# Kernel tuning notes

Measured on AMD Instinct MI355X. Metric: run time of the kernel, lower is better.

## Reference

```python
import jax, jax.numpy as jnp
import numpy as np

H, B, M, D = 2, 2048, 64, 16
N_ENT, N_REL = 500000, 32


def setup_inputs() -> dict:
    key = jax.random.key(0)
    k1, k2, k3, k4, k5, k6 = jax.random.split(key, 6)
    items = jax.random.randint(k1, (B,), 0, N_ENT)
    heads = jax.random.randint(k2, (H, B, M), 0, N_ENT)
    relations = jax.random.randint(k3, (H, B, M), 0, N_REL)
    tails = jax.random.randint(k4, (H, B, M), 0, N_ENT)
    ent_emb = jax.random.normal(k5, (N_ENT, D), dtype=jnp.float32) * 0.1
    rel_emb = jax.random.normal(k6, (N_REL, D, D), dtype=jnp.float32) * 0.1
    return {"items": items, "heads": heads, "relations": relations,
            "tails": tails, "ent_emb": ent_emb, "rel_emb": rel_emb}


def reference(items, heads, relations, tails, ent_emb, rel_emb):
    # gathers over ragged-as-dense ripple sets
    item_e = ent_emb[items]        # [B, D]
    head_e = ent_emb[heads]        # [H, B, M, D]
    rel_e = rel_emb[relations]     # [H, B, M, D, D]
    tail_e = ent_emb[tails]        # [H, B, M, D]
    # Rh = R @ h  -> [H, B, M, D]
    Rh = jnp.einsum('hbmij,hbmj->hbmi', rel_e, head_e)
    # attention logits hRv = Rh . v (item embedding) -> [H, B, M]
    hRv = jnp.einsum('hbmi,bi->hbm', Rh, item_e)
    pi = jax.nn.softmax(hRv, axis=2)          # softmax over memory dim (dim=1 in torch per hop)
    # weighted tail aggregation, summed over hops -> [B, D]
    user_rep = jnp.einsum('hbm,hbmd->bd', pi, tail_e)
    predicts = jax.nn.sigmoid(jnp.sum(user_rep * item_e, axis=1))  # [B]
    return predicts
```

## Files before the change

### kernel.cpp

```cpp
#include <hip/hip_runtime.h>
#include <math.h>

#define HOPS 2
#define BATCH 2048
#define MEM 64
#define DIM 16
#define NREL 32
#define RSTRIDE 20

__global__ __launch_bounds__(512)
void ripple_kernel(const int* __restrict__ items,
                   const int* __restrict__ heads,
                   const int* __restrict__ relations,
                   const int* __restrict__ tails,
                   const float* __restrict__ ent_emb,
                   const float* __restrict__ rel_emb,
                   float* __restrict__ out)
{
    const int b    = blockIdx.x;
    const int tid  = threadIdx.x;
    const int sub  = tid & 3;
    const int g    = tid >> 2;
    const int h    = g >> 6;
    const int m    = g & 63;
    const int wave = tid >> 6;

    __shared__ float s_itemR[NREL * RSTRIDE];
    __shared__ float s_num[8];
    __shared__ float s_den[8];

    const int base = h * (BATCH * MEM) + b * MEM + m;
    const int hidx = heads[base];
    const int ridx = relations[base];
    const int tidx = tails[base];

    const float4* ip = (const float4*)(ent_emb + (size_t)items[b] * DIM);
    const float4 it0 = ip[0], it1 = ip[1], it2 = ip[2], it3 = ip[3];

    const float4 hseg = *(const float4*)(ent_emb + (size_t)hidx * DIM + sub * 4);
    const float4 tseg = *(const float4*)(ent_emb + (size_t)tidx * DIM + sub * 4);

    {
        const int r = tid >> 4;
        const int j = tid & 15;
        const float* Rp = rel_emb + r * (DIM * DIM) + j;
        float acc;
        acc = it0.x * Rp[0];
        acc = fmaf(it0.y, Rp[16],  acc);
        acc = fmaf(it0.z, Rp[32],  acc);
        acc = fmaf(it0.w, Rp[48],  acc);
        acc = fmaf(it1.x, Rp[64],  acc);
        acc = fmaf(it1.y, Rp[80],  acc);
        acc = fmaf(it1.z, Rp[96],  acc);
        acc = fmaf(it1.w, Rp[112], acc);
        acc = fmaf(it2.x, Rp[128], acc);
        acc = fmaf(it2.y, Rp[144], acc);
        acc = fmaf(it2.z, Rp[160], acc);
        acc = fmaf(it2.w, Rp[176], acc);
        acc = fmaf(it3.x, Rp[192], acc);
        acc = fmaf(it3.y, Rp[208], acc);
        acc = fmaf(it3.z, Rp[224], acc);
        acc = fmaf(it3.w, Rp[240], acc);
        s_itemR[r * RSTRIDE + j] = acc;
    }
    __syncthreads();

    const float4 irseg = *(const float4*)(s_itemR + ridx * RSTRIDE + sub * 4);
    const float4 iseg  = (sub == 0) ? it0 : (sub == 1) ? it1
                       : (sub == 2) ? it2 : it3;

    float lpart = hseg.x * irseg.x + hseg.y * irseg.y +
                  hseg.z * irseg.z + hseg.w * irseg.w;
    float tpart = tseg.x * iseg.x + tseg.y * iseg.y +
                  tseg.z * iseg.z + tseg.w * iseg.w;

    lpart += __shfl_xor(lpart, 1, 64);
    lpart += __shfl_xor(lpart, 2, 64);

    const float e = __expf(lpart);
    float num = e * tpart;
    float den = e * 0.25f;
    #pragma unroll
    for (int off = 1; off < 64; off <<= 1) {
        num += __shfl_xor(num, off, 64);
        den += __shfl_xor(den, off, 64);
    }
    if ((tid & 63) == 0) { s_num[wave] = num; s_den[wave] = den; }
    __syncthreads();

    if (tid == 0) {
        const float n0 = s_num[0] + s_num[1] + s_num[2] + s_num[3];
        const float d0 = s_den[0] + s_den[1] + s_den[2] + s_den[3];
        const float n1 = s_num[4] + s_num[5] + s_num[6] + s_num[7];
        const float d1 = s_den[4] + s_den[5] + s_den[6] + s_den[7];
        const float x = n0 / d0 + n1 / d1;
        out[b] = 1.0f / (1.0f + __expf(-x));
    }
}

extern "C" void kernel_launch(void* const* d_in, const int* in_sizes, int n_in,
                              void* d_out, int out_size, void* d_ws, size_t ws_size,
                              hipStream_t stream) {
    const int*   items     = (const int*)d_in[0];
    const int*   heads     = (const int*)d_in[1];
    const int*   relations = (const int*)d_in[2];
    const int*   tails     = (const int*)d_in[3];
    const float* ent_emb   = (const float*)d_in[4];
    const float* rel_emb   = (const float*)d_in[5];
    float*       out       = (float*)d_out;

    ripple_kernel<<<BATCH, 512, 0, stream>>>(items, heads, relations, tails,
                                             ent_emb, rel_emb, out);
}
```

Measured before the change: 90.30 us.

## Process two batch rows per block to reuse relation matrix loads

```diff
diff --git a/kernel.cpp b/kernel.cpp
--- a/kernel.cpp
+++ b/kernel.cpp
@@ -8,7 +8,7 @@
 #define NREL 32
 #define RSTRIDE 20
 
-__global__ __launch_bounds__(512)
+__global__ __launch_bounds__(512, 4)
 void ripple_kernel(const int* __restrict__ items,
                    const int* __restrict__ heads,
                    const int* __restrict__ relations,
@@ -17,7 +17,8 @@
                    const float* __restrict__ rel_emb,
                    float* __restrict__ out)
 {
-    const int b    = blockIdx.x;
+    const int b0   = blockIdx.x * 2;
+    const int b1   = b0 + 1;
     const int tid  = threadIdx.x;
     const int sub  = tid & 3;
     const int g    = tid >> 2;
@@ -25,76 +26,111 @@
     const int m    = g & 63;
     const int wave = tid >> 6;
 
-    __shared__ float s_itemR[NREL * RSTRIDE];
-    __shared__ float s_num[8];
-    __shared__ float s_den[8];
+    __shared__ float s_itemR0[NREL * RSTRIDE];
+    __shared__ float s_itemR1[NREL * RSTRIDE];
+    __shared__ float s_num[2][8];
+    __shared__ float s_den[2][8];
 
-    const int base = h * (BATCH * MEM) + b * MEM + m;
-    const int hidx = heads[base];
-    const int ridx = relations[base];
-    const int tidx = tails[base];
+    const int base  = h * (BATCH * MEM) + m;
+    const int hidx0 = heads    [base + b0 * MEM];
+    const int ridx0 = relations[base + b0 * MEM];
+    const int tidx0 = tails    [base + b0 * MEM];
+    const int hidx1 = heads    [base + b1 * MEM];
+    const int ridx1 = relations[base + b1 * MEM];
+    const int tidx1 = tails    [base + b1 * MEM];
 
-    const float4* ip = (const float4*)(ent_emb + (size_t)items[b] * DIM);
-    const float4 it0 = ip[0], it1 = ip[1], it2 = ip[2], it3 = ip[3];
+    const float4* ip0 = (const float4*)(ent_emb + (size_t)items[b0] * DIM);
+    const float4* ip1 = (const float4*)(ent_emb + (size_t)items[b1] * DIM);
+    const float4 i00 = ip0[0], i01 = ip0[1], i02 = ip0[2], i03 = ip0[3];
+    const float4 i10 = ip1[0], i11 = ip1[1], i12 = ip1[2], i13 = ip1[3];
 
-    const float4 hseg = *(const float4*)(ent_emb + (size_t)hidx * DIM + sub * 4);
-    const float4 tseg = *(const float4*)(ent_emb + (size_t)tidx * DIM + sub * 4);
+    const int r = tid >> 4;
+    const int j = tid & 15;
+    const float* Rp = rel_emb + r * (DIM * DIM) + j;
+    float rp[16];
+    #pragma unroll
+    for (int i = 0; i < 16; ++i) rp[i] = Rp[i * 16];
+
+    const float4 h0seg = *(const float4*)(ent_emb + (size_t)hidx0 * DIM + sub * 4);
+    const float4 t0seg = *(const float4*)(ent_emb + (size_t)tidx0 * DIM + sub * 4);
+    const float4 h1seg = *(const float4*)(ent_emb + (size_t)hidx1 * DIM + sub * 4);
+    const float4 t1seg = *(const float4*)(ent_emb + (size_t)tidx1 * DIM + sub * 4);
 
     {
-        const int r = tid >> 4;
-        const int j = tid & 15;
-        const float* Rp = rel_emb + r * (DIM * DIM) + j;
-        float acc;
-        acc = it0.x * Rp[0];
-        acc = fmaf(it0.y, Rp[16],  acc);
-        acc = fmaf(it0.z, Rp[32],  acc);
-        acc = fmaf(it0.w, Rp[48],  acc);
-        acc = fmaf(it1.x, Rp[64],  acc);
-        acc = fmaf(it1.y, Rp[80],  acc);
-        acc = fmaf(it1.z, Rp[96],  acc);
-        acc = fmaf(it1.w, Rp[112], acc);
-        acc = fmaf(it2.x, Rp[128], acc);
-        acc = fmaf(it2.y, Rp[144], acc);
-        acc = fmaf(it2.z, Rp[160], acc);
-        acc = fmaf(it2.w, Rp[176], acc);
-        acc = fmaf(it3.x, Rp[192], acc);
-        acc = fmaf(it3.y, Rp[208], acc);
-        acc = fmaf(it3.z, Rp[224], acc);
-        acc = fmaf(it3.w, Rp[240], acc);
-        s_itemR[r * RSTRIDE + j] = acc;
+        float a0, a1;
+        a0 = i00.x * rp[0];          a1 = i10.x * rp[0];
+        a0 = fmaf(i00.y, rp[1],  a0); a1 = fmaf(i10.y, rp[1],  a1);
+        a0 = fmaf(i00.z, rp[2],  a0); a1 = fmaf(i10.z, rp[2],  a1);
+        a0 = fmaf(i00.w, rp[3],  a0); a1 = fmaf(i10.w, rp[3],  a1);
+        a0 = fmaf(i01.x, rp[4],  a0); a1 = fmaf(i11.x, rp[4],  a1);
+        a0 = fmaf(i01.y, rp[5],  a0); a1 = fmaf(i11.y, rp[5],  a1);
+        a0 = fmaf(i01.z, rp[6],  a0); a1 = fmaf(i11.z, rp[6],  a1);
+        a0 = fmaf(i01.w, rp[7],  a0); a1 = fmaf(i11.w, rp[7],  a1);
+        a0 = fmaf(i02.x, rp[8],  a0); a1 = fmaf(i12.x, rp[8],  a1);
+        a0 = fmaf(i02.y, rp[9],  a0); a1 = fmaf(i12.y, rp[9],  a1);
+        a0 = fmaf(i02.z, rp[10], a0); a1 = fmaf(i12.z, rp[10], a1);
+        a0 = fmaf(i02.w, rp[11], a0); a1 = fmaf(i12.w, rp[11], a1);
+        a0 = fmaf(i03.x, rp[12], a0); a1 = fmaf(i13.x, rp[12], a1);
+        a0 = fmaf(i03.y, rp[13], a0); a1 = fmaf(i13.y, rp[13], a1);
+        a0 = fmaf(i03.z, rp[14], a0); a1 = fmaf(i13.z, rp[14], a1);
+        a0 = fmaf(i03.w, rp[15], a0); a1 = fmaf(i13.w, rp[15], a1);
+        s_itemR0[r * RSTRIDE + j] = a0;
+        s_itemR1[r * RSTRIDE + j] = a1;
+    }
+
+    const float4 is0 = (sub == 0) ? i00 : (sub == 1) ? i01
+                     : (sub == 2) ? i02 : i03;
+    const float4 is1 = (sub == 0) ? i10 : (sub == 1) ? i11
+                     : (sub == 2) ? i12 : i13;
+    float tpart0 = t0seg.x * is0.x + t0seg.y * is0.y +
+                   t0seg.z * is0.z + t0seg.w * is0.w;
+    float tpart1 = t1seg.x * is1.x + t1seg.y * is1.y +
+                   t1seg.z * is1.z + t1seg.w * is1.w;
+
+    __syncthreads();
+
+    const float4 ir0 = *(const float4*)(s_itemR0 + ridx0 * RSTRIDE + sub * 4);
+    const float4 ir1 = *(const float4*)(s_itemR1 + ridx1 * RSTRIDE + sub * 4);
+
+    float l0 = h0seg.x * ir0.x + h0seg.y * ir0.y +
+               h0seg.z * ir0.z + h0seg.w * ir0.w;
+    float l1 = h1seg.x * ir1.x + h1seg.y * ir1.y +
+               h1seg.z * ir1.z + h1seg.w * ir1.w;
+
+    l0 += __shfl_xor(l0, 1, 64);
+    l0 += __shfl_xor(l0, 2, 64);
+    l1 += __shfl_xor(l1, 1, 64);
+    l1 += __shfl_xor(l1, 2, 64);
+
+    const float e0 = __expf(l0);
+    const float e1 = __expf(l1);
+    float num0 = e0 * tpart0;
+    float den0 = e0 * 0.25f;
+    float num1 = e1 * tpart1;
+    float den1 = e1 * 0.25f;
+    #pragma unroll
+    for (int off = 1; off < 64; off <<= 1) {
+        num0 += __shfl_xor(num0, off, 64);
+        den0 += __shfl_xor(den0, off, 64);
+        num1 += __shfl_xor(num1, off, 64);
+        den1 += __shfl_xor(den1, off, 64);
+    }
+    if ((tid & 63) == 0) {
+        s_num[0][wave] = num0; s_den[0][wave] = den0;
+        s_num[1][wave] = num1; s_den[1][wave] = den1;
     }
     __syncthreads();
 
-    const float4 irseg = *(const float4*)(s_itemR + ridx * RSTRIDE + sub * 4);
-    const float4 iseg  = (sub == 0) ? it0 : (sub == 1) ? it1
-                       : (sub == 2) ? it2 : it3;
-
-    float lpart = hseg.x * irseg.x + hseg.y * irseg.y +
-                  hseg.z * irseg.z + hseg.w * irseg.w;
-    float tpart = tseg.x * iseg.x + tseg.y * iseg.y +
-                  tseg.z * iseg.z + tseg.w * iseg.w;
-
-    lpart += __shfl_xor(lpart, 1, 64);
-    lpart += __shfl_xor(lpart, 2, 64);
-
-    const float e = __expf(lpart);
-    float num = e * tpart;
-    float den = e * 0.25f;
-    #pragma unroll
-    for (int off = 1; off < 64; off <<= 1) {
-        num += __shfl_xor(num, off, 64);
-        den += __shfl_xor(den, off, 64);
-    }
-    if ((tid & 63) == 0) { s_num[wave] = num; s_den[wave] = den; }
-    __syncthreads();
-
-    if (tid == 0) {
-        const float n0 = s_num[0] + s_num[1] + s_num[2] + s_num[3];
-        const float d0 = s_den[0] + s_den[1] + s_den[2] + s_den[3];
-        const float n1 = s_num[4] + s_num[5] + s_num[6] + s_num[7];
-        const float d1 = s_den[4] + s_den[5] + s_den[6] + s_den[7];
+    if ((tid & 255) == 0) {
+        const int bb = tid >> 8;
+        const float* nn = s_num[bb];
+        const float* dd = s_den[bb];
+        const float n0 = nn[0] + nn[1] + nn[2] + nn[3];
+        const float d0 = dd[0] + dd[1] + dd[2] + dd[3];
+        const float n1 = nn[4] + nn[5] + nn[6] + nn[7];
+        const float d1 = dd[4] + dd[5] + dd[6] + dd[7];
         const float x = n0 / d0 + n1 / d1;
-        out[b] = 1.0f / (1.0f + __expf(-x));
+        out[b0 + bb] = 1.0f / (1.0f + __expf(-x));
     }
 }
 
@@ -109,6 +145,6 @@
     const float* rel_emb   = (const float*)d_in[5];
     float*       out       = (float*)d_out;
 
-    ripple_kernel<<<BATCH, 512, 0, stream>>>(items, heads, relations, tails,
-                                             ent_emb, rel_emb, out);
+    ripple_kernel<<<BATCH / 2, 512, 0, stream>>>(items, heads, relations, tails,
+                                                 ent_emb, rel_emb, out);
 }
```

New measurement: 89.03 us. Within noise of the previous version (-1.4%).
